# Performance work log

Measured on AMD Instinct MI355X. Metric: run time of the kernel, lower is better.

## Reference

```python
import jax, jax.numpy as jnp
import numpy as np

B, S, D = 2, 2048, 1024          # batch, seq, n_embd
E, GS, K = 8, 4, 2               # num_experts, group_size, top-k
H = 2 * D                        # hidden_dim of SharedExpertMLP
A = H // 16                      # adapt_dim = 128
G = E // GS                      # num_groups
LN_EPS = 1e-5


def _ln(z, g, b):
    mu = jnp.mean(z, -1, keepdims=True)
    v = jnp.mean((z - mu) ** 2, -1, keepdims=True)
    return (z - mu) * jax.lax.rsqrt(v + LN_EPS) * g + b


def setup_inputs() -> dict:
    key = jax.random.key(0)
    ks = jax.random.split(key, 12)
    s = float(D) ** -0.5
    sa = s * 0.01
    se = 0.01 * float(A) ** -0.5
    n = lambda k, shape, std: jax.random.normal(k, shape, jnp.float32) * std
    return {
        'x': jax.random.normal(ks[0], (B, S, D), jnp.float32),
        'W_up': n(ks[1], (H, D), s),
        'W_gate': n(ks[2], (H, D), s),
        'W_down': n(ks[3], (D, H), s),
        'W_pre': n(ks[4], (A, D), sa),
        'W_post': n(ks[5], (A, H), sa),
        'ln_g': jnp.ones((A,), jnp.float32),
        'ln_b': jnp.zeros((A,), jnp.float32),
        'W_aproj': n(ks[6], (H, A), sa),
        'A_exp': n(ks[7], (E, A, A), se),
        'ln_g_e': jnp.ones((E, A), jnp.float32),
        'ln_b_e': jnp.zeros((E, A), jnp.float32),
        'W_eproj': n(ks[8], (H, A), se),
        'W_oproj': n(ks[9], (D, H), se),
        'W_rg': n(ks[10], (G, D), 0.001),
        'W_re': n(ks[11], (GS, D), 0.001),
    }


def reference(x, W_up, W_gate, W_down, W_pre, W_post, ln_g, ln_b, W_aproj,
              A_exp, ln_g_e, ln_b_e, W_eproj, W_oproj, W_rg, W_re):
    silu = jax.nn.silu
    # ---- SharedExpertMLP ----
    up = x @ W_up.T
    gate = x @ W_gate.T
    hidden = silu(gate) * up                               # [B,S,H]
    adapt_in = _ln(x @ W_pre.T, ln_g, ln_b)                # [B,S,A]
    adapt_out = _ln(hidden @ W_post.T, ln_g, ln_b)         # [B,S,A]
    aw = silu(jnp.clip(jnp.einsum('bsa,bta->bst', adapt_in, adapt_out), -5.0, 5.0))
    adapt = jnp.einsum('bst,bta->bsa', aw, adapt_in)
    hidden = hidden + 0.1 * (adapt @ W_aproj.T)
    shared = hidden @ W_down.T                             # [B,S,D]
    # ---- HierarchicalRouter ----
    gl = x @ W_rg.T                                        # [B,S,G]
    gp = jax.nn.softmax(gl, -1)
    gw = jnp.max(gp, -1)                                   # top-1 group weight
    gidx = jnp.argmax(gp, -1)
    el = x @ W_re.T                                        # [B,S,GS]
    ep = jax.nn.softmax(el, -1)
    wloc, iloc = jax.lax.top_k(ep, K)
    eidx = gidx[..., None] * GS + iloc                     # [B,S,K] global expert ids
    wloc = wloc / (jnp.sum(wloc, -1, keepdims=True) + 1e-7)
    fw = gw[..., None] * wloc                              # final weights
    N = B * S
    dm = jnp.zeros((N, E), x.dtype).at[
        jnp.arange(N)[:, None], eidx.reshape(N, K)].set(fw.reshape(N, K))
    load = dm.sum(0)
    target = load.sum() / E
    router_loss = 0.001 * (jnp.mean((load - target) ** 2)
                           + jnp.mean(gl ** 2) + jnp.mean(el ** 2))
    dm = dm.reshape(B, S, E)
    # ---- ExpertGroup combine (vectorized masked gather/MLP/scatter) ----
    pre = x @ W_pre.T                                      # [B,S,A]
    h_e = jnp.einsum('bsa,eca->ebsc', pre, A_exp)          # per-expert adapter
    h_e = _ln(h_e, ln_g_e[:, None, None, :], ln_b_e[:, None, None, :])
    contrib = jnp.einsum('ebsc,hc->ebsh', h_e, W_eproj)    # [E,B,S,H]
    contrib = jnp.einsum('ebsh,dh->ebsd', contrib, W_oproj)
    w_e = jnp.moveaxis(dm, -1, 0)                          # [E,B,S]
    out = jnp.sum(dm, -1)[..., None] * shared + 0.1 * jnp.einsum('ebsd,ebs->bsd', contrib, w_e)
    return out, router_loss
```

## Files before the change

### kernel.cpp

```cpp
#include <hip/hip_runtime.h>
#include <hip/hip_bf16.h>
#include <math.h>

static constexpr int Bc = 2;
static constexpr int Sc = 2048;
static constexpr int Dc = 1024;
static constexpr int Hc = 2048;
static constexpr int Ac = 128;
static constexpr int Ec = 8;
static constexpr int GSc = 4;
static constexpr int Gc = 2;
static constexpr int Nc = Bc * Sc;
static constexpr float LN_EPSc = 1e-5f;
static constexpr int RBLK = 512;

typedef __attribute__((ext_vector_type(8))) short bf16x8;
typedef __attribute__((ext_vector_type(4))) float f32x4;
typedef __attribute__((ext_vector_type(4))) unsigned short us4;

__device__ __forceinline__ unsigned short f2b(float f) {
    union { float f; unsigned u; } v; v.f = f;
    return (unsigned short)((v.u + 0x7FFFu + ((v.u >> 16) & 1u)) >> 16);
}
__device__ __forceinline__ float b2f(unsigned short h) {
    union { unsigned u; float f; } v; v.u = (unsigned)h << 16; return v.f;
}
__device__ __forceinline__ float fsilu(float x) {
    return x / (1.f + __expf(-x));
}

#define GLOAD16(g, l) __builtin_amdgcn_global_load_lds( \
    (const __attribute__((address_space(1))) void*)(g), \
    (__attribute__((address_space(3))) void*)(l), 16, 0, 0)

template<int EPI>
__global__ __launch_bounds__(256, 4) void mgemm(
    const unsigned short* __restrict__ Ag, const unsigned short* __restrict__ Bg,
    void* __restrict__ Cg, int N, int K, int lda, int ldb, float alpha,
    float* __restrict__ aux, void* __restrict__ aux2,
    long long sA, long long sB, long long sC)
{
    __shared__ unsigned short As[128 * 64];
    __shared__ unsigned short Bs[128 * 64];
    const unsigned short* A = Ag + (long long)blockIdx.z * sA;
    const unsigned short* B = Bg + (long long)blockIdx.z * sB;
    float* fC = (float*)Cg + (long long)blockIdx.z * sC;
    unsigned short* usC = (unsigned short*)Cg + (long long)blockIdx.z * sC;

    const int nwg = gridDim.x * gridDim.y;
    const int flat = blockIdx.y * gridDim.x + blockIdx.x;
    const int swz = (flat & 7) * (nwg >> 3) + (flat >> 3);
    const int bx = swz % gridDim.x, by = swz / gridDim.x;
    const int bm = by * 128, bn = bx * 128;

    const int tid = threadIdx.x;
    const int w = tid >> 6, l = tid & 63;
    const int wm = (w >> 1) * 64, wn = (w & 1) * 64;
    const int fr = l & 15, g = l >> 4;

    const f32x4 zero = { 0.f, 0.f, 0.f, 0.f };
    f32x4 acc[4][4];
    #pragma unroll
    for (int i = 0; i < 4; ++i)
        #pragma unroll
        for (int j = 0; j < 4; ++j) acc[i][j] = zero;

    for (int k0 = 0; k0 < K; k0 += 64) {
        #pragma unroll
        for (int p = 0; p < 4; ++p) {
            const int c = p * 256 + tid;
            const int row = c >> 3;
            const int gch = (c & 7) ^ ((c >> 4) & 7);
            GLOAD16(A + (long long)(bm + row) * lda + k0 + gch * 8, &As[c * 8]);
            GLOAD16(B + (long long)(bn + row) * ldb + k0 + gch * 8, &Bs[c * 8]);
        }
        __syncthreads();
        #pragma unroll
        for (int h = 0; h < 2; ++h) {
            bf16x8 af[4], bfv[4];
            #pragma unroll
            for (int i = 0; i < 4; ++i) {
                const int ra = wm + i * 16 + fr;
                af[i]  = *(const bf16x8*)&As[ra * 64 + ((h * 4 + g) ^ ((ra >> 1) & 7)) * 8];
                const int rb = wn + i * 16 + fr;
                bfv[i] = *(const bf16x8*)&Bs[rb * 64 + ((h * 4 + g) ^ ((rb >> 1) & 7)) * 8];
            }
            #pragma unroll
            for (int i = 0; i < 4; ++i)
                #pragma unroll
                for (int j = 0; j < 4; ++j)
                    acc[i][j] = __builtin_amdgcn_mfma_f32_16x16x32_bf16(af[i], bfv[j], acc[i][j], 0, 0, 0);
        }
        __syncthreads();
    }

    if (EPI == 9) {
        if (bn < 2 * Hc) {
            #pragma unroll
            for (int mi = 0; mi < 4; ++mi) {
                #pragma unroll
                for (int j = 0; j < 2; ++j) {
                    #pragma unroll
                    for (int jr = 0; jr < 4; ++jr) {
                        const long long row = bm + wm + mi * 16 + g * 4 + jr;
                        const long long colh = ((bn + wn) >> 1) + j * 16 + fr;
                        const float gv = acc[mi][2 * j][jr];
                        const float uv = acc[mi][2 * j + 1][jr];
                        usC[row * Hc + colh] = f2b(fsilu(gv) * uv);
                    }
                }
            }
        } else {
            unsigned short* preb = (unsigned short*)aux2;
            #pragma unroll
            for (int mi = 0; mi < 4; ++mi) {
                #pragma unroll
                for (int ni = 0; ni < 4; ++ni) {
                    #pragma unroll
                    for (int jr = 0; jr < 4; ++jr) {
                        const long long row = bm + wm + mi * 16 + g * 4 + jr;
                        const int lc = wn + ni * 16 + fr;
                        const float v = acc[mi][ni][jr];
                        aux[row * Ac + lc] = v;
                        preb[row * Ac + lc] = f2b(v);
                    }
                }
            }
        }
    } else {
        #pragma unroll
        for (int mi = 0; mi < 4; ++mi)
            #pragma unroll
            for (int ni = 0; ni < 4; ++ni)
                #pragma unroll
                for (int jr = 0; jr < 4; ++jr) {
                    const long long row = bm + wm + mi * 16 + g * 4 + jr;
                    const long long col = bn + wn + ni * 16 + fr;
                    const long long idx = row * (long long)N + col;
                    const float v = acc[mi][ni][jr];
                    if (EPI == 0) fC[idx] = v;
                    else usC[idx] = f2b(alpha * v);
                }
    }
}

__global__ __launch_bounds__(256, 2) void mgemm64(
    const unsigned short* __restrict__ Ag, const unsigned short* __restrict__ Bg,
    float* __restrict__ Cg, int N, int K, int lda, int ldb, int zmod,
    long long sA1, long long sB1, long long sC1,
    long long sA2, long long sB2, long long sC2)
{
    __shared__ unsigned short As[128 * 32];
    __shared__ unsigned short Bs[64 * 32];
    const int z1 = blockIdx.z % zmod, z2 = blockIdx.z / zmod;
    const unsigned short* A = Ag + (long long)z1 * sA1 + (long long)z2 * sA2;
    const unsigned short* B = Bg + (long long)z1 * sB1 + (long long)z2 * sB2;
    float* fC = Cg + (long long)z1 * sC1 + (long long)z2 * sC2;

    const int nwg = gridDim.x * gridDim.y;
    const int flat = blockIdx.y * gridDim.x + blockIdx.x;
    const int swz = (flat & 7) * (nwg >> 3) + (flat >> 3);
    const int bx = swz % gridDim.x, by = swz / gridDim.x;
    const int bm = by * 128, bn = bx * 64;

    const int tid = threadIdx.x;
    const int w = tid >> 6, l = tid & 63;
    const int wm = (w >> 1) * 64, wn = (w & 1) * 32;
    const int fr = l & 15, g = l >> 4;

    const f32x4 zero = { 0.f, 0.f, 0.f, 0.f };
    f32x4 acc[4][2];
    #pragma unroll
    for (int i = 0; i < 4; ++i)
        #pragma unroll
        for (int j = 0; j < 2; ++j) acc[i][j] = zero;

    for (int k0 = 0; k0 < K; k0 += 32) {
        #pragma unroll
        for (int p = 0; p < 2; ++p) {
            const int c = p * 256 + tid;
            GLOAD16(A + (long long)(bm + (c >> 2)) * lda + k0 + (c & 3) * 8, &As[c * 8]);
        }
        GLOAD16(B + (long long)(bn + (tid >> 2)) * ldb + k0 + (tid & 3) * 8, &Bs[tid * 8]);
        __syncthreads();
        bf16x8 af[4], bfv[2];
        #pragma unroll
        for (int i = 0; i < 4; ++i)
            af[i]  = *(const bf16x8*)&As[(wm + i * 16 + fr) * 32 + g * 8];
        #pragma unroll
        for (int j = 0; j < 2; ++j)
            bfv[j] = *(const bf16x8*)&Bs[(wn + j * 16 + fr) * 32 + g * 8];
        #pragma unroll
        for (int i = 0; i < 4; ++i)
            #pragma unroll
            for (int j = 0; j < 2; ++j)
                acc[i][j] = __builtin_amdgcn_mfma_f32_16x16x32_bf16(af[i], bfv[j], acc[i][j], 0, 0, 0);
        __syncthreads();
    }

    #pragma unroll
    for (int mi = 0; mi < 4; ++mi)
        #pragma unroll
        for (int ni = 0; ni < 2; ++ni)
            #pragma unroll
            for (int jr = 0; jr < 4; ++jr) {
                const long long row = bm + wm + mi * 16 + g * 4 + jr;
                const long long col = bn + wn + ni * 16 + fr;
                fC[row * (long long)N + col] = acc[mi][ni][jr];
            }
}

__global__ __launch_bounds__(256, 2) void fadapt_k(
    const unsigned short* __restrict__ adapt_in,
    const unsigned short* __restrict__ adapt_out,
    const unsigned short* __restrict__ adapt_inT,
    float* __restrict__ partial)
{
    __shared__ unsigned short P_lds[4 * 128 * 32];
    __shared__ unsigned short Bs[128 * 32];

    const int b = blockIdx.z;
    const int q0 = blockIdx.y * 128;
    const int t0 = blockIdx.x * 256;

    const unsigned short* Qg = adapt_in + (long long)b * Sc * Ac;
    const unsigned short* Kg = adapt_out + (long long)b * Sc * Ac;
    const unsigned short* Vt = adapt_inT + (long long)b * Ac * Sc;

    const int tid = threadIdx.x;
    const int w = tid >> 6, l = tid & 63;
    const int wm = (w >> 1) * 64, wn = (w & 1) * 64;
    const int fr = l & 15, g = l >> 4;

    bf16x8 qf[4][4];
    for (int ks = 0; ks < 4; ++ks) {
        #pragma unroll
        for (int p = 0; p < 2; ++p) {
            const int c = p * 256 + tid;
            GLOAD16(Qg + (long long)(q0 + (c >> 2)) * Ac + ks * 32 + (c & 3) * 8, &Bs[c * 8]);
        }
        __syncthreads();
        #pragma unroll
        for (int i = 0; i < 4; ++i)
            qf[i][ks] = *(const bf16x8*)&Bs[(wm + i * 16 + fr) * 32 + g * 8];
        __syncthreads();
    }

    const f32x4 zero = { 0.f, 0.f, 0.f, 0.f };
    f32x4 acc[4][4];
    #pragma unroll
    for (int i = 0; i < 4; ++i)
        #pragma unroll
        for (int j = 0; j < 4; ++j) acc[i][j] = zero;

    #pragma unroll 1
    for (int ts = 0; ts < 2; ++ts) {
        const int t1 = t0 + ts * 128;
        f32x4 sacc[4][4];
        #pragma unroll
        for (int i = 0; i < 4; ++i)
            #pragma unroll
            for (int j = 0; j < 4; ++j) sacc[i][j] = zero;
        for (int ks = 0; ks < 4; ++ks) {
            #pragma unroll
            for (int p = 0; p < 2; ++p) {
                const int c = p * 256 + tid;
                GLOAD16(Kg + (long long)(t1 + (c >> 2)) * Ac + ks * 32 + (c & 3) * 8, &Bs[c * 8]);
            }
            __syncthreads();
            bf16x8 bfv[4];
            #pragma unroll
            for (int j = 0; j < 4; ++j)
                bfv[j] = *(const bf16x8*)&Bs[(wn + j * 16 + fr) * 32 + g * 8];
            #pragma unroll
            for (int i = 0; i < 4; ++i)
                #pragma unroll
                for (int j = 0; j < 4; ++j)
                    sacc[i][j] = __builtin_amdgcn_mfma_f32_16x16x32_bf16(qf[i][ks], bfv[j], sacc[i][j], 0, 0, 0);
            __syncthreads();
        }
        #pragma unroll
        for (int mi = 0; mi < 4; ++mi) {
            #pragma unroll
            for (int ni = 0; ni < 4; ++ni) {
                const int t = wn + ni * 16 + fr;
                const int base = (t >> 5) * 4096 + (t & 31);
                #pragma unroll
                for (int jr = 0; jr < 4; ++jr) {
                    const int row = wm + mi * 16 + g * 4 + jr;
                    float v = sacc[mi][ni][jr];
                    v = fminf(fmaxf(v, -5.f), 5.f);
                    P_lds[base + row * 32] = f2b(fsilu(v));
                }
            }
        }
        __syncthreads();
        for (int ks = 0; ks < 4; ++ks) {
            #pragma unroll
            for (int p = 0; p < 2; ++p) {
                const int c = p * 256 + tid;
                GLOAD16(Vt + (long long)(c >> 2) * Sc + t1 + ks * 32 + (c & 3) * 8, &Bs[c * 8]);
            }
            __syncthreads();
            bf16x8 af[4], bfv[4];
            #pragma unroll
            for (int i = 0; i < 4; ++i)
                af[i] = *(const bf16x8*)&P_lds[ks * 4096 + (wm + i * 16 + fr) * 32 + g * 8];
            #pragma unroll
            for (int j = 0; j < 4; ++j)
                bfv[j] = *(const bf16x8*)&Bs[(wn + j * 16 + fr) * 32 + g * 8];
            #pragma unroll
            for (int i = 0; i < 4; ++i)
                #pragma unroll
                for (int j = 0; j < 4; ++j)
                    acc[i][j] = __builtin_amdgcn_mfma_f32_16x16x32_bf16(af[i], bfv[j], acc[i][j], 0, 0, 0);
            __syncthreads();
        }
    }

    float* op = partial + ((long long)blockIdx.x * Bc + b) * Sc * Ac;
    #pragma unroll
    for (int mi = 0; mi < 4; ++mi)
        #pragma unroll
        for (int ni = 0; ni < 4; ++ni)
            #pragma unroll
            for (int jr = 0; jr < 4; ++jr) {
                const long long row = q0 + wm + mi * 16 + g * 4 + jr;
                const long long col = wn + ni * 16 + fr;
                op[row * Ac + col] = acc[mi][ni][jr];
            }
}

__global__ __launch_bounds__(256, 2) void final_k(
    const unsigned short* __restrict__ hidden, const unsigned short* __restrict__ Wd,
    const unsigned short* __restrict__ adaptb, const unsigned short* __restrict__ Wdap,
    const unsigned short* __restrict__ h2v, const unsigned short* __restrict__ Wopep,
    const float* __restrict__ dmsum, float* __restrict__ out)
{
    __shared__ unsigned short As[128 * 64];
    __shared__ unsigned short Bs[64 * 64];

    const int nwg = gridDim.x * gridDim.y;
    const int flat = blockIdx.y * gridDim.x + blockIdx.x;
    const int swz = (flat & 7) * (nwg >> 3) + (flat >> 3);
    const int bx = swz % gridDim.x, by = swz / gridDim.x;
    const int bm = by * 128, bn = bx * 64;

    const int tid = threadIdx.x;
    const int w = tid >> 6, l = tid & 63;
    const int wm = (w >> 1) * 64, wn = (w & 1) * 32;
    const int fr = l & 15, g = l >> 4;

    const f32x4 zero = { 0.f, 0.f, 0.f, 0.f };
    f32x4 acc[4][2];
    #pragma unroll
    for (int i = 0; i < 4; ++i)
        #pragma unroll
        for (int j = 0; j < 2; ++j) acc[i][j] = zero;

    const unsigned short* Ap[3] = { hidden, adaptb, h2v };
    const unsigned short* Bp[3] = { Wd, Wdap, Wopep };
    const int Ks[3]  = { Hc, Ac, Ac };
    const int lds[3] = { Hc, Ac, Ac };

    #pragma unroll 1
    for (int ph = 0; ph < 3; ++ph) {
        if (ph == 2) {
            #pragma unroll
            for (int mi = 0; mi < 4; ++mi)
                #pragma unroll
                for (int jr = 0; jr < 4; ++jr) {
                    const float rs = dmsum[bm + wm + mi * 16 + g * 4 + jr];
                    #pragma unroll
                    for (int ni = 0; ni < 2; ++ni) acc[mi][ni][jr] *= rs;
                }
        }
        const unsigned short* A = Ap[ph];
        const unsigned short* B = Bp[ph];
        const int K = Ks[ph], ld = lds[ph];
        for (int k0 = 0; k0 < K; k0 += 64) {
            #pragma unroll
            for (int p = 0; p < 4; ++p) {
                const int c = p * 256 + tid;
                const int row = c >> 3;
                const int gch = (c & 7) ^ ((c >> 4) & 7);
                GLOAD16(A + (long long)(bm + row) * ld + k0 + gch * 8, &As[c * 8]);
            }
            #pragma unroll
            for (int p = 0; p < 2; ++p) {
                const int c = p * 256 + tid;
                const int row = c >> 3;
                const int gch = (c & 7) ^ ((c >> 4) & 7);
                GLOAD16(B + (long long)(bn + row) * ld + k0 + gch * 8, &Bs[c * 8]);
            }
            __syncthreads();
            #pragma unroll
            for (int h = 0; h < 2; ++h) {
                bf16x8 af[4], bfv[2];
                #pragma unroll
                for (int i = 0; i < 4; ++i) {
                    const int ra = wm + i * 16 + fr;
                    af[i]  = *(const bf16x8*)&As[ra * 64 + ((h * 4 + g) ^ ((ra >> 1) & 7)) * 8];
                }
                #pragma unroll
                for (int j = 0; j < 2; ++j) {
                    const int rb = wn + j * 16 + fr;
                    bfv[j] = *(const bf16x8*)&Bs[rb * 64 + ((h * 4 + g) ^ ((rb >> 1) & 7)) * 8];
                }
                #pragma unroll
                for (int i = 0; i < 4; ++i)
                    #pragma unroll
                    for (int j = 0; j < 2; ++j)
                        acc[i][j] = __builtin_amdgcn_mfma_f32_16x16x32_bf16(af[i], bfv[j], acc[i][j], 0, 0, 0);
            }
            __syncthreads();
        }
    }

    #pragma unroll
    for (int mi = 0; mi < 4; ++mi)
        #pragma unroll
        for (int ni = 0; ni < 2; ++ni)
            #pragma unroll
            for (int jr = 0; jr < 4; ++jr) {
                const long long row = bm + wm + mi * 16 + g * 4 + jr;
                const long long col = bn + wn + ni * 16 + fr;
                out[row * (long long)Dc + col] = acc[mi][ni][jr];
            }
}

template<int NP, int BF>
__global__ __launch_bounds__(256) void reduce_k(const float* __restrict__ in,
                                                void* __restrict__ outp,
                                                long long pstride, int n4, float alpha)
{
    for (int i = blockIdx.x * 256 + threadIdx.x; i < n4; i += gridDim.x * 256) {
        float4 s = ((const float4*)in)[i];
        #pragma unroll
        for (int p = 1; p < NP; ++p) {
            const float4 v = ((const float4*)(in + (long long)p * pstride))[i];
            s.x += v.x; s.y += v.y; s.z += v.z; s.w += v.w;
        }
        s.x *= alpha; s.y *= alpha; s.z *= alpha; s.w *= alpha;
        if (BF) {
            us4 o = { f2b(s.x), f2b(s.y), f2b(s.z), f2b(s.w) };
            ((us4*)outp)[i] = o;
        } else {
            ((float4*)outp)[i] = s;
        }
    }
}

struct PrepArgs {
    const float* csrc[4]; unsigned short* cdst[4]; int cn4[4];
    const float* Wg; const float* Wu; const float* Wpre; unsigned short* Wcat;
    const float* tin0; const float* tin1; unsigned short* tout0; unsigned short* tout1;
};
__global__ __launch_bounds__(256) void prep_k(PrepArgs a)
{
    __shared__ float T[64][68];
    const int y = blockIdx.y;
    if (y < 4) {
        const float4* s = (const float4*)a.csrc[y];
        us4* d = (us4*)a.cdst[y];
        const int n = a.cn4[y];
        for (int i = blockIdx.x * 256 + threadIdx.x; i < n; i += gridDim.x * 256) {
            const float4 v = s[i];
            us4 o;
            o.x = f2b(v.x); o.y = f2b(v.y); o.z = f2b(v.z); o.w = f2b(v.w);
            d[i] = o;
        }
    } else if (y == 4) {
        const int total = (2 * Hc + Ac) * 256;
        for (int u = blockIdx.x * 256 + threadIdx.x; u < total; u += gridDim.x * 256) {
            const int r = u >> 8, t = u & 255;
            const float* src; int srcrow;
            if (r < 2 * Hc) {
                const int b = r >> 5, wq = r & 31;
                src = (wq < 16) ? a.Wg : a.Wu;
                srcrow = b * 16 + (wq & 15);
            } else {
                src = a.Wpre;
                srcrow = r - 2 * Hc;
            }
            const float4 v = ((const float4*)(src + (long long)srcrow * Dc))[t];
            us4 o;
            o.x = f2b(v.x); o.y = f2b(v.y); o.z = f2b(v.z); o.w = f2b(v.w);
            ((us4*)(a.Wcat + (long long)r * Dc))[t] = o;
        }
    } else {
        const int rr = threadIdx.x >> 4, cc = (threadIdx.x & 15) * 4;
        for (int tb = blockIdx.x; tb < 128; tb += gridDim.x) {
            const int z = tb >> 6, rem = tb & 63;
            const int a0 = (rem >> 5) * 64, t0 = (rem & 31) * 64;
            const float* in = z ? a.tin1 : a.tin0;
            unsigned short* outp = z ? a.tout1 : a.tout0;
            __syncthreads();
            #pragma unroll
            for (int p = 0; p < 4; ++p) {
                const int row = p * 16 + rr;
                *(float4*)&T[row][cc] = *(const float4*)&in[(long long)(t0 + row) * Ac + a0 + cc];
            }
            __syncthreads();
            #pragma unroll
            for (int p = 0; p < 4; ++p) {
                const int ar = p * 16 + rr;
                us4 o;
                o.x = f2b(T[cc + 0][ar]); o.y = f2b(T[cc + 1][ar]);
                o.z = f2b(T[cc + 2][ar]); o.w = f2b(T[cc + 3][ar]);
                *(us4*)&outp[(long long)(a0 + ar) * Hc + t0 + cc] = o;
            }
        }
    }
}

__global__ __launch_bounds__(256) void lntr_k(const float* __restrict__ in,
                                              unsigned short* __restrict__ outn,
                                              unsigned short* __restrict__ outt,
                                              const float* __restrict__ gg,
                                              const float* __restrict__ bb)
{
    __shared__ unsigned short L[64][130];
    const int z = blockIdx.y;
    const int t0 = blockIdx.x * 64;
    const int wv = threadIdx.x >> 6, lane = threadIdx.x & 63;
    const float g0 = gg[lane], g1 = gg[lane + 64];
    const float b0 = bb[lane], b1 = bb[lane + 64];

    #pragma unroll 4
    for (int it = 0; it < 16; ++it) {
        const int row = wv * 16 + it;
        const long long gr = (long long)(z * Sc + t0 + row) * 128;
        const float z0 = in[gr + lane], z1 = in[gr + 64 + lane];
        float s = z0 + z1;
        #pragma unroll
        for (int o = 32; o > 0; o >>= 1) s += __shfl_xor(s, o, 64);
        const float mu = s * (1.f / 128.f);
        const float d0 = z0 - mu, d1 = z1 - mu;
        float v = d0 * d0 + d1 * d1;
        #pragma unroll
        for (int o = 32; o > 0; o >>= 1) v += __shfl_xor(v, o, 64);
        const float r = rsqrtf(v * (1.f / 128.f) + LN_EPSc);
        L[row][lane] = f2b(d0 * r * g0 + b0);
        L[row][lane + 64] = f2b(d1 * r * g1 + b1);
    }
    __syncthreads();
    {
        const int row = threadIdx.x >> 2, seg = (threadIdx.x & 3) * 32;
        #pragma unroll
        for (int j = 0; j < 8; ++j)
            *(us4*)&outn[(long long)(z * Sc + t0 + row) * 128 + seg + j * 4] =
                *(const us4*)&L[row][seg + j * 4];
    }
    {
        const int a = threadIdx.x >> 1, tt0 = (threadIdx.x & 1) * 32;
        #pragma unroll
        for (int j4 = 0; j4 < 8; ++j4) {
            us4 o;
            o.x = L[tt0 + j4 * 4 + 0][a]; o.y = L[tt0 + j4 * 4 + 1][a];
            o.z = L[tt0 + j4 * 4 + 2][a]; o.w = L[tt0 + j4 * 4 + 3][a];
            *(us4*)&outt[(long long)z * Ac * Sc + (long long)a * Sc + t0 + tt0 + j4 * 4] = o;
        }
    }
}

__global__ __launch_bounds__(64) void redln_k(const float* __restrict__ in,
                                              unsigned short* __restrict__ out,
                                              const float* __restrict__ gg,
                                              const float* __restrict__ bb,
                                              long long pstride)
{
    const int row = blockIdx.x;
    const int lane = threadIdx.x;
    float z0 = 0.f, z1 = 0.f;
    #pragma unroll
    for (int p = 0; p < 4; ++p) {
        z0 += in[p * pstride + (long long)row * 128 + lane];
        z1 += in[p * pstride + (long long)row * 128 + 64 + lane];
    }
    float s = z0 + z1;
    for (int o = 32; o > 0; o >>= 1) s += __shfl_xor(s, o, 64);
    const float mu = s * (1.f / 128.f);
    const float d0 = z0 - mu, d1 = z1 - mu;
    float v = d0 * d0 + d1 * d1;
    for (int o = 32; o > 0; o >>= 1) v += __shfl_xor(v, o, 64);
    const float r = rsqrtf(v * (1.f / 128.f) + LN_EPSc);
    out[(long long)row * 128 + lane] = f2b(d0 * r * gg[lane] + bb[lane]);
    out[(long long)row * 128 + 64 + lane] = f2b(d1 * r * gg[lane + 64] + bb[lane + 64]);
}

__global__ __launch_bounds__(256) void router_k(const float* __restrict__ x,
                                                const float* __restrict__ W_rg,
                                                const float* __restrict__ W_re,
                                                int* __restrict__ eidx, float* __restrict__ fw,
                                                float* __restrict__ dmsum,
                                                float* __restrict__ rpart,
                                                unsigned short* __restrict__ xb)
{
    const int wv = threadIdx.x >> 6;
    const int lane = threadIdx.x & 63;
    float load8[8] = {0.f, 0.f, 0.f, 0.f, 0.f, 0.f, 0.f, 0.f};
    float sqg = 0.f, sqe = 0.f;

    #pragma unroll
    for (int it = 0; it < 2; ++it) {
        const int t = blockIdx.x * 8 + wv * 2 + it;
        const float* xr = x + (long long)t * Dc;
        float a0 = 0, a1 = 0, a2 = 0, a3 = 0, a4 = 0, a5 = 0;
        #pragma unroll
        for (int j = 0; j < 16; ++j) {
            const int d = lane + 64 * j;
            const float xv = xr[d];
            xb[(long long)t * Dc + d] = f2b(xv);
            a0 += xv * W_rg[d];          a1 += xv * W_rg[Dc + d];
            a2 += xv * W_re[d];          a3 += xv * W_re[Dc + d];
            a4 += xv * W_re[2 * Dc + d]; a5 += xv * W_re[3 * Dc + d];
        }
        #pragma unroll
        for (int o = 32; o > 0; o >>= 1) {
            a0 += __shfl_xor(a0, o, 64); a1 += __shfl_xor(a1, o, 64);
            a2 += __shfl_xor(a2, o, 64); a3 += __shfl_xor(a3, o, 64);
            a4 += __shfl_xor(a4, o, 64); a5 += __shfl_xor(a5, o, 64);
        }
        if (lane == 0) {
            const float gl0 = a0, gl1 = a1;
            const float m = fmaxf(gl0, gl1);
            const float e0 = expf(gl0 - m), e1 = expf(gl1 - m);
            const float inv = 1.f / (e0 + e1);
            const float gp0 = e0 * inv, gp1 = e1 * inv;
            const int gidx = (gl1 > gl0) ? 1 : 0;
            const float gw = fmaxf(gp0, gp1);
            float el[4] = { a2, a3, a4, a5 };
            const float me = fmaxf(fmaxf(el[0], el[1]), fmaxf(el[2], el[3]));
            float ep[4]; float se = 0.f;
            #pragma unroll
            for (int i = 0; i < 4; ++i) { ep[i] = expf(el[i] - me); se += ep[i]; }
            const float invs = 1.f / se;
            #pragma unroll
            for (int i = 0; i < 4; ++i) ep[i] *= invs;
            int i0 = 0;
            #pragma unroll
            for (int i = 1; i < 4; ++i) if (ep[i] > ep[i0]) i0 = i;
            int i1 = -1;
            #pragma unroll
            for (int i = 0; i < 4; ++i) { if (i == i0) continue; if (i1 < 0 || ep[i] > ep[i1]) i1 = i; }
            const float w0 = ep[i0], w1 = ep[i1];
            const float sn = w0 + w1 + 1e-7f;
            const float f0 = gw * w0 / sn, f1 = gw * w1 / sn;
            const int ei0 = gidx * GSc + i0, ei1 = gidx * GSc + i1;
            eidx[t * 2] = ei0; eidx[t * 2 + 1] = ei1;
            fw[t * 2] = f0; fw[t * 2 + 1] = f1;
            dmsum[t] = f0 + f1;
            #pragma unroll
            for (int e = 0; e < 8; ++e)
                load8[e] += ((e == ei0) ? f0 : 0.f) + ((e == ei1) ? f1 : 0.f);
            sqg += gl0 * gl0 + gl1 * gl1;
            sqe += el[0] * el[0] + el[1] * el[1] + el[2] * el[2] + el[3] * el[3];
        }
    }
    __shared__ float sh[4][10];
    if (lane == 0) {
        #pragma unroll
        for (int e = 0; e < 8; ++e) sh[wv][e] = load8[e];
        sh[wv][8] = sqg; sh[wv][9] = sqe;
    }
    __syncthreads();
    if (threadIdx.x < 10) {
        rpart[blockIdx.x * 10 + threadIdx.x] =
            sh[0][threadIdx.x] + sh[1][threadIdx.x] + sh[2][threadIdx.x] + sh[3][threadIdx.x];
    }
}

__global__ __launch_bounds__(512) void loss_k(const float* __restrict__ rpart,
                                              float* __restrict__ out_loss)
{
    const int tid = threadIdx.x;
    const int lane = tid & 63, wv = tid >> 6;
    float v[10];
    #pragma unroll
    for (int c = 0; c < 10; ++c) v[c] = rpart[tid * 10 + c];
    #pragma unroll
    for (int o = 32; o > 0; o >>= 1)
        #pragma unroll
        for (int c = 0; c < 10; ++c) v[c] += __shfl_xor(v[c], o, 64);
    __shared__ float sh[8][10];
    if (lane == 0) {
        #pragma unroll
        for (int c = 0; c < 10; ++c) sh[wv][c] = v[c];
    }
    __syncthreads();
    if (tid == 0) {
        float load[8]; float sqg = 0.f, sqe = 0.f;
        #pragma unroll
        for (int e = 0; e < 8; ++e) load[e] = 0.f;
        for (int wvi = 0; wvi < 8; ++wvi) {
            #pragma unroll
            for (int e = 0; e < 8; ++e) load[e] += sh[wvi][e];
            sqg += sh[wvi][8]; sqe += sh[wvi][9];
        }
        float s = 0.f;
        for (int e = 0; e < Ec; ++e) s += load[e];
        const float tgt = s / (float)Ec;
        float var = 0.f;
        for (int e = 0; e < Ec; ++e) { const float d = load[e] - tgt; var += d * d; }
        var /= (float)Ec;
        const float l = var + sqg / (float)(Nc * Gc) + sqe / (float)(Nc * GSc);
        *out_loss = 0.001f * l;
    }
}

__global__ __launch_bounds__(128) void combine_k(const float* __restrict__ h_dense,
                                                 const float* __restrict__ ln_g_e,
                                                 const float* __restrict__ ln_b_e,
                                                 const int* __restrict__ eidx,
                                                 const float* __restrict__ fw,
                                                 unsigned short* __restrict__ h2)
{
    const int t = blockIdx.x;
    const int tid = threadIdx.x;
    __shared__ float red[2];

    float acc = 0.f;
    #pragma unroll
    for (int slot = 0; slot < 2; ++slot) {
        const int e = eidx[t * 2 + slot];
        const float w = fw[t * 2 + slot];
        const float h = h_dense[((long long)e * Nc + t) * 128 + tid];
        float v = h;
        for (int o = 32; o > 0; o >>= 1) v += __shfl_down(v, o, 64);
        if ((tid & 63) == 0) red[tid >> 6] = v;
        __syncthreads();
        const float mu = (red[0] + red[1]) * (1.f / 128.f);
        __syncthreads();
        const float d = h - mu;
        v = d * d;
        for (int o = 32; o > 0; o >>= 1) v += __shfl_down(v, o, 64);
        if ((tid & 63) == 0) red[tid >> 6] = v;
        __syncthreads();
        const float var = (red[0] + red[1]) * (1.f / 128.f);
        __syncthreads();
        acc += w * (d * rsqrtf(var + LN_EPSc) * ln_g_e[e * 128 + tid] + ln_b_e[e * 128 + tid]);
    }
    h2[(long long)t * 128 + tid] = f2b(acc);
}

extern "C" void kernel_launch(void* const* d_in, const int* in_sizes, int n_in,
                              void* d_out, int out_size, void* d_ws, size_t ws_size,
                              hipStream_t stream)
{
    const float* x       = (const float*)d_in[0];
    const float* W_up    = (const float*)d_in[1];
    const float* W_gate  = (const float*)d_in[2];
    const float* W_down  = (const float*)d_in[3];
    const float* W_pre   = (const float*)d_in[4];
    const float* W_post  = (const float*)d_in[5];
    const float* ln_g    = (const float*)d_in[6];
    const float* ln_b    = (const float*)d_in[7];
    const float* W_aproj = (const float*)d_in[8];
    const float* A_exp   = (const float*)d_in[9];
    const float* ln_g_e  = (const float*)d_in[10];
    const float* ln_b_e  = (const float*)d_in[11];
    const float* W_eproj = (const float*)d_in[12];
    const float* W_oproj = (const float*)d_in[13];
    const float* W_rg    = (const float*)d_in[14];
    const float* W_re    = (const float*)d_in[15];

    float* out = (float*)d_out;

    char* p = (char*)d_ws;
    auto alloc = [&](size_t bytes) { void* r = (void*)p; p += (bytes + 255) & ~(size_t)255; return r; };
    float* pre      = (float*)alloc((size_t)Nc * Ac * 4);
    float* h_dense  = (float*)alloc((size_t)Ec * Nc * Ac * 4);
    float* rpart    = (float*)alloc((size_t)RBLK * 10 * 4);
    float* fw       = (float*)alloc((size_t)Nc * 2 * 4);
    float* dmsum    = (float*)alloc((size_t)Nc * 4);
    int*   eidx     = (int*)alloc((size_t)Nc * 2 * 4);
    unsigned short* xb      = (unsigned short*)alloc((size_t)Nc * Dc * 2);
    unsigned short* Wcat_b  = (unsigned short*)alloc((size_t)(2 * Hc + Ac) * Dc * 2);
    unsigned short* Wd_b    = (unsigned short*)alloc((size_t)Dc * Hc * 2);
    unsigned short* Wop_b   = (unsigned short*)alloc((size_t)Dc * Hc * 2);
    unsigned short* Wpost_b = (unsigned short*)alloc((size_t)Ac * Hc * 2);
    unsigned short* WapT_b  = (unsigned short*)alloc((size_t)Ac * Hc * 2);
    unsigned short* WepT_b  = (unsigned short*)alloc((size_t)Ac * Hc * 2);
    unsigned short* Wdap_b  = (unsigned short*)alloc((size_t)Dc * Ac * 2);
    unsigned short* Wopep_b = (unsigned short*)alloc((size_t)Dc * Ac * 2);
    unsigned short* Aexp_b  = (unsigned short*)alloc((size_t)Ec * Ac * Ac * 2);
    unsigned short* pre_b   = (unsigned short*)alloc((size_t)Nc * Ac * 2);
    unsigned short* hidden  = (unsigned short*)alloc((size_t)Nc * Hc * 2);
    unsigned short* adapt_in  = (unsigned short*)alloc((size_t)Nc * Ac * 2);
    unsigned short* adapt_inT = (unsigned short*)alloc((size_t)Nc * Ac * 2);
    unsigned short* adapt_out = (unsigned short*)alloc((size_t)Nc * Ac * 2);
    unsigned short* adaptb    = (unsigned short*)alloc((size_t)Nc * Ac * 2);
    unsigned short* h2        = (unsigned short*)alloc((size_t)Nc * Ac * 2);

    float* wprepP = h_dense;
    float* postP  = h_dense;
    float* adaptP = h_dense;

    PrepArgs pa;
    pa.csrc[0] = W_down;  pa.cdst[0] = Wd_b;    pa.cn4[0] = Dc * Hc / 4;
    pa.csrc[1] = W_oproj; pa.cdst[1] = Wop_b;   pa.cn4[1] = Dc * Hc / 4;
    pa.csrc[2] = W_post;  pa.cdst[2] = Wpost_b; pa.cn4[2] = Ac * Hc / 4;
    pa.csrc[3] = A_exp;   pa.cdst[3] = Aexp_b;  pa.cn4[3] = Ec * Ac * Ac / 4;
    pa.Wg = W_gate; pa.Wu = W_up; pa.Wpre = W_pre; pa.Wcat = Wcat_b;
    pa.tin0 = W_aproj; pa.tin1 = W_eproj; pa.tout0 = WapT_b; pa.tout1 = WepT_b;
    prep_k<<<dim3(64, 6), 256, 0, stream>>>(pa);

    router_k<<<RBLK, 256, 0, stream>>>(x, W_rg, W_re, eidx, fw, dmsum, rpart, xb);
    loss_k<<<1, 512, 0, stream>>>(rpart, out + (size_t)Nc * Dc);

    mgemm64<<<dim3(2, 8, 8), 256, 0, stream>>>(Wd_b, WapT_b, wprepP, Ac, 512, Hc, Hc,
        2,
        (long long)Dc * Hc, (long long)Ac * Hc, (long long)Dc * Ac,
        512, 512, (long long)2 * Dc * Ac);
    reduce_k<4, 1><<<256, 256, 0, stream>>>(wprepP, Wdap_b,
        (long long)2 * Dc * Ac, 2 * Dc * Ac / 4, 0.1f);

    mgemm<9><<<dim3(33, 32), 256, 0, stream>>>(xb, Wcat_b, hidden, 2 * Hc + Ac, Dc, Dc, Dc, 0.f,
        pre, pre_b, 0, 0, 0);
    lntr_k<<<dim3(Sc / 64, Bc), 256, 0, stream>>>(pre, adapt_in, adapt_inT, ln_g, ln_b);

    mgemm64<<<dim3(2, 32, 4), 256, 0, stream>>>(hidden, Wpost_b, postP, Ac, 512, Hc, Hc,
        8, 512, 512, (long long)Nc * Ac, 0, 0, 0);
    redln_k<<<Nc, 64, 0, stream>>>(postP, adapt_out, ln_g, ln_b, (long long)Nc * Ac);

    mgemm64<<<dim3(2, 32, Ec), 256, 0, stream>>>(pre_b, Aexp_b, h_dense, Ac, Ac, Ac, Ac,
        16, 0, (long long)Ac * Ac, (long long)Nc * Ac, 0, 0, 0);
    combine_k<<<Nc, 128, 0, stream>>>(h_dense, ln_g_e, ln_b_e, eidx, fw, h2);

    fadapt_k<<<dim3(8, 16, 2), 256, 0, stream>>>(adapt_in, adapt_out, adapt_inT, adaptP);
    reduce_k<8, 1><<<512, 256, 0, stream>>>(adaptP, adaptb,
        (long long)2 * Sc * Ac, 2 * Sc * Ac / 4, 1.f);

    final_k<<<dim3(Dc / 64, Nc / 128), 256, 0, stream>>>(
        hidden, Wd_b, adaptb, Wdap_b, h2, Wopep_b, dmsum, out);
}
```

Before: 198.1 us.

## Double-buffer LDS tiles with async prefetch across all GEMM kernels

Converts the mgemm, mgemm64, attention-style and final GEMM kernels from single-buffered K-loops to double-buffered ones. The next K-slice is issued with global_load_lds while MFMAs run on the current buffer, removing one barrier per iteration. Tile depth drops from 64 to 32 to keep LDS usage flat, and XOR swizzles are added to the 32-wide tiles and P_lds to cut bank conflicts. final_k's occupancy hint rises to 4; the risk is that a prefetch of only 32 K-columns may be too short to hide memory latency, and more loop iterations add overhead.

```diff
diff --git a/kernel.cpp b/kernel.cpp
--- a/kernel.cpp
+++ b/kernel.cpp
@@ -33,6 +33,7 @@
     (const __attribute__((address_space(1))) void*)(g), \
     (__attribute__((address_space(3))) void*)(l), 16, 0, 0)
 
+
 template<int EPI>
 __global__ __launch_bounds__(256, 4) void mgemm(
     const unsigned short* __restrict__ Ag, const unsigned short* __restrict__ Bg,
@@ -40,8 +41,8 @@
     float* __restrict__ aux, void* __restrict__ aux2,
     long long sA, long long sB, long long sC)
 {
-    __shared__ unsigned short As[128 * 64];
-    __shared__ unsigned short Bs[128 * 64];
+    __shared__ unsigned short As[2][128 * 32];
+    __shared__ unsigned short Bs[2][128 * 32];
     const unsigned short* A = Ag + (long long)blockIdx.z * sA;
     const unsigned short* B = Bg + (long long)blockIdx.z * sB;
     float* fC = (float*)Cg + (long long)blockIdx.z * sC;
@@ -65,33 +66,38 @@
         #pragma unroll
         for (int j = 0; j < 4; ++j) acc[i][j] = zero;
 
-    for (int k0 = 0; k0 < K; k0 += 64) {
-        #pragma unroll
-        for (int p = 0; p < 4; ++p) {
+    auto stage = [&](int k0, int buf) {
+        #pragma unroll
+        for (int p = 0; p < 2; ++p) {
             const int c = p * 256 + tid;
-            const int row = c >> 3;
-            const int gch = (c & 7) ^ ((c >> 4) & 7);
-            GLOAD16(A + (long long)(bm + row) * lda + k0 + gch * 8, &As[c * 8]);
-            GLOAD16(B + (long long)(bn + row) * ldb + k0 + gch * 8, &Bs[c * 8]);
-        }
-        __syncthreads();
-        #pragma unroll
-        for (int h = 0; h < 2; ++h) {
-            bf16x8 af[4], bfv[4];
-            #pragma unroll
-            for (int i = 0; i < 4; ++i) {
-                const int ra = wm + i * 16 + fr;
-                af[i]  = *(const bf16x8*)&As[ra * 64 + ((h * 4 + g) ^ ((ra >> 1) & 7)) * 8];
-                const int rb = wn + i * 16 + fr;
-                bfv[i] = *(const bf16x8*)&Bs[rb * 64 + ((h * 4 + g) ^ ((rb >> 1) & 7)) * 8];
-            }
-            #pragma unroll
-            for (int i = 0; i < 4; ++i)
-                #pragma unroll
-                for (int j = 0; j < 4; ++j)
-                    acc[i][j] = __builtin_amdgcn_mfma_f32_16x16x32_bf16(af[i], bfv[j], acc[i][j], 0, 0, 0);
-        }
-        __syncthreads();
+            const int row = c >> 2;
+            const int gch = (c & 3) ^ ((row >> 1) & 3);
+            GLOAD16(A + (long long)(bm + row) * lda + k0 + gch * 8, &As[buf][c * 8]);
+            GLOAD16(B + (long long)(bn + row) * ldb + k0 + gch * 8, &Bs[buf][c * 8]);
+        }
+    };
+
+    stage(0, 0);
+    __syncthreads();
+    int cur = 0;
+    const int nk = K >> 5;
+    for (int t = 0; t < nk; ++t) {
+        if (t + 1 < nk) stage((t + 1) << 5, cur ^ 1);
+        bf16x8 af[4], bfv[4];
+        #pragma unroll
+        for (int i = 0; i < 4; ++i) {
+            const int ra = wm + i * 16 + fr;
+            af[i]  = *(const bf16x8*)&As[cur][ra * 32 + (g ^ ((ra >> 1) & 3)) * 8];
+            const int rb = wn + i * 16 + fr;
+            bfv[i] = *(const bf16x8*)&Bs[cur][rb * 32 + (g ^ ((rb >> 1) & 3)) * 8];
+        }
+        #pragma unroll
+        for (int i = 0; i < 4; ++i)
+            #pragma unroll
+            for (int j = 0; j < 4; ++j)
+                acc[i][j] = __builtin_amdgcn_mfma_f32_16x16x32_bf16(af[i], bfv[j], acc[i][j], 0, 0, 0);
+        __syncthreads();
+        cur ^= 1;
     }
 
     if (EPI == 9) {
@@ -150,8 +156,8 @@
     long long sA1, long long sB1, long long sC1,
     long long sA2, long long sB2, long long sC2)
 {
-    __shared__ unsigned short As[128 * 32];
-    __shared__ unsigned short Bs[64 * 32];
+    __shared__ unsigned short As[2][128 * 32];
+    __shared__ unsigned short Bs[2][64 * 32];
     const int z1 = blockIdx.z % zmod, z2 = blockIdx.z / zmod;
     const unsigned short* A = Ag + (long long)z1 * sA1 + (long long)z2 * sA2;
     const unsigned short* B = Bg + (long long)z1 * sB1 + (long long)z2 * sB2;
@@ -175,27 +181,46 @@
         #pragma unroll
         for (int j = 0; j < 2; ++j) acc[i][j] = zero;
 
-    for (int k0 = 0; k0 < K; k0 += 32) {
+    auto stage = [&](int k0, int buf) {
         #pragma unroll
         for (int p = 0; p < 2; ++p) {
             const int c = p * 256 + tid;
-            GLOAD16(A + (long long)(bm + (c >> 2)) * lda + k0 + (c & 3) * 8, &As[c * 8]);
-        }
-        GLOAD16(B + (long long)(bn + (tid >> 2)) * ldb + k0 + (tid & 3) * 8, &Bs[tid * 8]);
-        __syncthreads();
+            const int row = c >> 2;
+            const int gch = (c & 3) ^ ((row >> 1) & 3);
+            GLOAD16(A + (long long)(bm + row) * lda + k0 + gch * 8, &As[buf][c * 8]);
+        }
+        {
+            const int c = tid;
+            const int row = c >> 2;
+            const int gch = (c & 3) ^ ((row >> 1) & 3);
+            GLOAD16(B + (long long)(bn + row) * ldb + k0 + gch * 8, &Bs[buf][c * 8]);
+        }
+    };
+
+    stage(0, 0);
+    __syncthreads();
+    int cur = 0;
+    const int nk = K >> 5;
+    for (int t = 0; t < nk; ++t) {
+        if (t + 1 < nk) stage((t + 1) << 5, cur ^ 1);
         bf16x8 af[4], bfv[2];
         #pragma unroll
-        for (int i = 0; i < 4; ++i)
-            af[i]  = *(const bf16x8*)&As[(wm + i * 16 + fr) * 32 + g * 8];
-        #pragma unroll
-        for (int j = 0; j < 2; ++j)
-            bfv[j] = *(const bf16x8*)&Bs[(wn + j * 16 + fr) * 32 + g * 8];
+        for (int i = 0; i < 4; ++i) {
+            const int ra = wm + i * 16 + fr;
+            af[i]  = *(const bf16x8*)&As[cur][ra * 32 + (g ^ ((ra >> 1) & 3)) * 8];
+        }
+        #pragma unroll
+        for (int j = 0; j < 2; ++j) {
+            const int rb = wn + j * 16 + fr;
+            bfv[j] = *(const bf16x8*)&Bs[cur][rb * 32 + (g ^ ((rb >> 1) & 3)) * 8];
+        }
         #pragma unroll
         for (int i = 0; i < 4; ++i)
             #pragma unroll
             for (int j = 0; j < 2; ++j)
                 acc[i][j] = __builtin_amdgcn_mfma_f32_16x16x32_bf16(af[i], bfv[j], acc[i][j], 0, 0, 0);
         __syncthreads();
+        cur ^= 1;
     }
 
     #pragma unroll
@@ -217,7 +242,7 @@
     float* __restrict__ partial)
 {
     __shared__ unsigned short P_lds[4 * 128 * 32];
-    __shared__ unsigned short Bs[128 * 32];
+    __shared__ unsigned short Bs[2][128 * 32];
 
     const int b = blockIdx.z;
     const int q0 = blockIdx.y * 128;
@@ -232,18 +257,47 @@
     const int wm = (w >> 1) * 64, wn = (w & 1) * 64;
     const int fr = l & 15, g = l >> 4;
 
-    bf16x8 qf[4][4];
-    for (int ks = 0; ks < 4; ++ks) {
+    auto stageQ = [&](int ks, int buf) {
         #pragma unroll
         for (int p = 0; p < 2; ++p) {
             const int c = p * 256 + tid;
-            GLOAD16(Qg + (long long)(q0 + (c >> 2)) * Ac + ks * 32 + (c & 3) * 8, &Bs[c * 8]);
-        }
-        __syncthreads();
-        #pragma unroll
-        for (int i = 0; i < 4; ++i)
-            qf[i][ks] = *(const bf16x8*)&Bs[(wm + i * 16 + fr) * 32 + g * 8];
-        __syncthreads();
+            const int row = c >> 2;
+            const int gch = (c & 3) ^ ((row >> 1) & 3);
+            GLOAD16(Qg + (long long)(q0 + row) * Ac + ks * 32 + gch * 8, &Bs[buf][c * 8]);
+        }
+    };
+    auto stageK = [&](int t1, int ks, int buf) {
+        #pragma unroll
+        for (int p = 0; p < 2; ++p) {
+            const int c = p * 256 + tid;
+            const int row = c >> 2;
+            const int gch = (c & 3) ^ ((row >> 1) & 3);
+            GLOAD16(Kg + (long long)(t1 + row) * Ac + ks * 32 + gch * 8, &Bs[buf][c * 8]);
+        }
+    };
+    auto stageV = [&](int t1, int ks, int buf) {
+        #pragma unroll
+        for (int p = 0; p < 2; ++p) {
+            const int c = p * 256 + tid;
+            const int row = c >> 2;
+            const int gch = (c & 3) ^ ((row >> 1) & 3);
+            GLOAD16(Vt + (long long)row * Sc + t1 + ks * 32 + gch * 8, &Bs[buf][c * 8]);
+        }
+    };
+
+    bf16x8 qf[4][4];
+    stageQ(0, 0);
+    __syncthreads();
+    int cur = 0;
+    for (int ks = 0; ks < 4; ++ks) {
+        if (ks < 3) stageQ(ks + 1, cur ^ 1);
+        #pragma unroll
+        for (int i = 0; i < 4; ++i) {
+            const int ra = wm + i * 16 + fr;
+            qf[i][ks] = *(const bf16x8*)&Bs[cur][ra * 32 + (g ^ ((ra >> 1) & 3)) * 8];
+        }
+        __syncthreads();
+        cur ^= 1;
     }
 
     const f32x4 zero = { 0.f, 0.f, 0.f, 0.f };
@@ -261,60 +315,63 @@
         for (int i = 0; i < 4; ++i)
             #pragma unroll
             for (int j = 0; j < 4; ++j) sacc[i][j] = zero;
+        stageK(t1, 0, cur);
+        __syncthreads();
         for (int ks = 0; ks < 4; ++ks) {
-            #pragma unroll
-            for (int p = 0; p < 2; ++p) {
-                const int c = p * 256 + tid;
-                GLOAD16(Kg + (long long)(t1 + (c >> 2)) * Ac + ks * 32 + (c & 3) * 8, &Bs[c * 8]);
-            }
-            __syncthreads();
+            if (ks < 3) stageK(t1, ks + 1, cur ^ 1);
             bf16x8 bfv[4];
             #pragma unroll
-            for (int j = 0; j < 4; ++j)
-                bfv[j] = *(const bf16x8*)&Bs[(wn + j * 16 + fr) * 32 + g * 8];
+            for (int j = 0; j < 4; ++j) {
+                const int rb = wn + j * 16 + fr;
+                bfv[j] = *(const bf16x8*)&Bs[cur][rb * 32 + (g ^ ((rb >> 1) & 3)) * 8];
+            }
             #pragma unroll
             for (int i = 0; i < 4; ++i)
                 #pragma unroll
                 for (int j = 0; j < 4; ++j)
                     sacc[i][j] = __builtin_amdgcn_mfma_f32_16x16x32_bf16(qf[i][ks], bfv[j], sacc[i][j], 0, 0, 0);
             __syncthreads();
-        }
+            cur ^= 1;
+        }
+        stageV(t1, 0, cur);
         #pragma unroll
         for (int mi = 0; mi < 4; ++mi) {
             #pragma unroll
             for (int ni = 0; ni < 4; ++ni) {
                 const int t = wn + ni * 16 + fr;
-                const int base = (t >> 5) * 4096 + (t & 31);
+                const int tl = t & 31;
+                const int kbase = (t >> 5) * 4096;
                 #pragma unroll
                 for (int jr = 0; jr < 4; ++jr) {
                     const int row = wm + mi * 16 + g * 4 + jr;
                     float v = sacc[mi][ni][jr];
                     v = fminf(fmaxf(v, -5.f), 5.f);
-                    P_lds[base + row * 32] = f2b(fsilu(v));
+                    const int pos = (((tl >> 3) ^ ((row >> 1) & 3)) << 3) + (tl & 7);
+                    P_lds[kbase + row * 32 + pos] = f2b(fsilu(v));
                 }
             }
         }
         __syncthreads();
         for (int ks = 0; ks < 4; ++ks) {
-            #pragma unroll
-            for (int p = 0; p < 2; ++p) {
-                const int c = p * 256 + tid;
-                GLOAD16(Vt + (long long)(c >> 2) * Sc + t1 + ks * 32 + (c & 3) * 8, &Bs[c * 8]);
-            }
-            __syncthreads();
+            if (ks < 3) stageV(t1, ks + 1, cur ^ 1);
             bf16x8 af[4], bfv[4];
             #pragma unroll
-            for (int i = 0; i < 4; ++i)
-                af[i] = *(const bf16x8*)&P_lds[ks * 4096 + (wm + i * 16 + fr) * 32 + g * 8];
-            #pragma unroll
-            for (int j = 0; j < 4; ++j)
-                bfv[j] = *(const bf16x8*)&Bs[(wn + j * 16 + fr) * 32 + g * 8];
+            for (int i = 0; i < 4; ++i) {
+                const int ra = wm + i * 16 + fr;
+                af[i] = *(const bf16x8*)&P_lds[ks * 4096 + ra * 32 + (g ^ ((ra >> 1) & 3)) * 8];
+            }
+            #pragma unroll
+            for (int j = 0; j < 4; ++j) {
+                const int rb = wn + j * 16 + fr;
+                bfv[j] = *(const bf16x8*)&Bs[cur][rb * 32 + (g ^ ((rb >> 1) & 3)) * 8];
+            }
             #pragma unroll
             for (int i = 0; i < 4; ++i)
                 #pragma unroll
                 for (int j = 0; j < 4; ++j)
                     acc[i][j] = __builtin_amdgcn_mfma_f32_16x16x32_bf16(af[i], bfv[j], acc[i][j], 0, 0, 0);
             __syncthreads();
+            cur ^= 1;
         }
     }
 
@@ -331,14 +388,14 @@
             }
 }
 
-__global__ __launch_bounds__(256, 2) void final_k(
+__global__ __launch_bounds__(256, 4) void final_k(
     const unsigned short* __restrict__ hidden, const unsigned short* __restrict__ Wd,
     const unsigned short* __restrict__ adaptb, const unsigned short* __restrict__ Wdap,
     const unsigned short* __restrict__ h2v, const unsigned short* __restrict__ Wopep,
     const float* __restrict__ dmsum, float* __restrict__ out)
 {
-    __shared__ unsigned short As[128 * 64];
-    __shared__ unsigned short Bs[64 * 64];
+    __shared__ unsigned short As[2][128 * 32];
+    __shared__ unsigned short Bs[2][64 * 32];
 
     const int nwg = gridDim.x * gridDim.y;
     const int flat = blockIdx.y * gridDim.x + blockIdx.x;
@@ -360,8 +417,7 @@
 
     const unsigned short* Ap[3] = { hidden, adaptb, h2v };
     const unsigned short* Bp[3] = { Wd, Wdap, Wopep };
-    const int Ks[3]  = { Hc, Ac, Ac };
-    const int lds[3] = { Hc, Ac, Ac };
+    const int Ks[3] = { Hc, Ac, Ac };
 
     #pragma unroll 1
     for (int ph = 0; ph < 3; ++ph) {
@@ -377,43 +433,48 @@
         }
         const unsigned short* A = Ap[ph];
         const unsigned short* B = Bp[ph];
-        const int K = Ks[ph], ld = lds[ph];
-        for (int k0 = 0; k0 < K; k0 += 64) {
-            #pragma unroll
-            for (int p = 0; p < 4; ++p) {
-                const int c = p * 256 + tid;
-                const int row = c >> 3;
-                const int gch = (c & 7) ^ ((c >> 4) & 7);
-                GLOAD16(A + (long long)(bm + row) * ld + k0 + gch * 8, &As[c * 8]);
-            }
+        const int K = Ks[ph];
+
+        auto stage = [&](int k0, int buf) {
             #pragma unroll
             for (int p = 0; p < 2; ++p) {
                 const int c = p * 256 + tid;
-                const int row = c >> 3;
-                const int gch = (c & 7) ^ ((c >> 4) & 7);
-                GLOAD16(B + (long long)(bn + row) * ld + k0 + gch * 8, &Bs[c * 8]);
-            }
+                const int row = c >> 2;
+                const int gch = (c & 3) ^ ((row >> 1) & 3);
+                GLOAD16(A + (long long)(bm + row) * K + k0 + gch * 8, &As[buf][c * 8]);
+            }
+            {
+                const int c = tid;
+                const int row = c >> 2;
+                const int gch = (c & 3) ^ ((row >> 1) & 3);
+                GLOAD16(B + (long long)(bn + row) * K + k0 + gch * 8, &Bs[buf][c * 8]);
+            }
+        };
+
+        stage(0, 0);
+        __syncthreads();
+        int cur = 0;
+        const int nk = K >> 5;
+        for (int t = 0; t < nk; ++t) {
+            if (t + 1 < nk) stage((t + 1) << 5, cur ^ 1);
+            bf16x8 af[4], bfv[2];
+            #pragma unroll
+            for (int i = 0; i < 4; ++i) {
+                const int ra = wm + i * 16 + fr;
+                af[i]  = *(const bf16x8*)&As[cur][ra * 32 + (g ^ ((ra >> 1) & 3)) * 8];
+            }
+            #pragma unroll
+            for (int j = 0; j < 2; ++j) {
+                const int rb = wn + j * 16 + fr;
+                bfv[j] = *(const bf16x8*)&Bs[cur][rb * 32 + (g ^ ((rb >> 1) & 3)) * 8];
+            }
+            #pragma unroll
+            for (int i = 0; i < 4; ++i)
+                #pragma unroll
+                for (int j = 0; j < 2; ++j)
+                    acc[i][j] = __builtin_amdgcn_mfma_f32_16x16x32_bf16(af[i], bfv[j], acc[i][j], 0, 0, 0);
             __syncthreads();
-            #pragma unroll
-            for (int h = 0; h < 2; ++h) {
-                bf16x8 af[4], bfv[2];
-                #pragma unroll
-                for (int i = 0; i < 4; ++i) {
-                    const int ra = wm + i * 16 + fr;
-                    af[i]  = *(const bf16x8*)&As[ra * 64 + ((h * 4 + g) ^ ((ra >> 1) & 7)) * 8];
-                }
-                #pragma unroll
-                for (int j = 0; j < 2; ++j) {
-                    const int rb = wn + j * 16 + fr;
-                    bfv[j] = *(const bf16x8*)&Bs[rb * 64 + ((h * 4 + g) ^ ((rb >> 1) & 7)) * 8];
-                }
-                #pragma unroll
-                for (int i = 0; i < 4; ++i)
-                    #pragma unroll
-                    for (int j = 0; j < 2; ++j)
-                        acc[i][j] = __builtin_amdgcn_mfma_f32_16x16x32_bf16(af[i], bfv[j], acc[i][j], 0, 0, 0);
-            }
-            __syncthreads();
+            cur ^= 1;
         }
     }
 
```

Result: slower. 232.3 us (+17.2%).
